# Kernel tuning notes

Hardware: AMD Instinct MI355X
Metric: run time of the kernel (lower is better)

Reference implementation:

```python
import jax, jax.numpy as jnp
import numpy as np

EPS = 1e-3  # kernel epsilon used in Performer generalized kernel
B, H, N, D, M = 1, 8, 1024, 64, 128  # batch, heads, seq, dim_heads, nb_features


def _gaussian_orthogonal_matrix(m, d, seed=0):
    # GaussianOrthogonalRandomMatrix with scaling=0: stacked QR blocks, rows
    # rescaled by chi-distributed norms of gaussian d-vectors.
    rng = np.random.default_rng(seed)
    blocks = []
    for _ in range(m // d):
        g = rng.standard_normal((d, d))
        qmat, _ = np.linalg.qr(g)
        blocks.append(qmat.T)
    proj = np.concatenate(blocks, axis=0)  # [m, d], orthonormal rows per block
    mult = np.linalg.norm(rng.standard_normal((m, d)), axis=1)  # chi norms
    return (mult[:, None] * proj).astype(np.float32)


def setup_inputs() -> dict:
    key = jax.random.key(0)
    kq, kk, kv = jax.random.split(key, 3)
    q = jax.random.normal(kq, (B, H, N, D), dtype=jnp.float32)
    k = jax.random.normal(kk, (B, H, N, D), dtype=jnp.float32)
    v = jax.random.normal(kv, (B, H, N, D), dtype=jnp.float32)
    proj = jnp.asarray(_gaussian_orthogonal_matrix(M, D))
    return {"q": q, "k": k, "v": v, "proj": proj}


def _generalized_kernel(x, proj):
    # kernel_fn(relu)( (x / d**0.25) @ proj^T ) + eps
    normalizer = 1.0 / (x.shape[-1] ** 0.25)
    xp = jnp.einsum('bhnd,md->bhnm', x * normalizer, proj)
    return jax.nn.relu(xp) + EPS


def reference(q, k, v, proj):
    qp = _generalized_kernel(q, proj)  # [B,H,N,M]
    kp = _generalized_kernel(k, proj)  # [B,H,N,M]
    # causal linear attention
    k_cumsum = jnp.cumsum(kp, axis=-2)                              # [B,H,N,M]
    context = jnp.einsum('bhnm,bhne->bhnme', kp, v)                 # [B,H,N,M,D]
    context = jnp.cumsum(context, axis=-3)                          # prefix sums over n
    context = context / k_cumsum[..., None]                         # normalize
    out = jnp.einsum('bhnme,bhnm->bhne', context, qp)               # [B,H,N,D]
    return out
```

## Files before the change

kernel.cpp:

```cpp
#include <hip/hip_runtime.h>

static constexpr int H = 8, N = 1024, D = 64, M = 128, CHUNK = 128, NC = 8;
static constexpr float EPS = 1e-3f;
static constexpr float NORM = 0.35355339059327373f;

typedef __attribute__((ext_vector_type(8))) short short8;
typedef __attribute__((ext_vector_type(4))) float f32x4;

__device__ inline unsigned short f2bf(float x) {
    unsigned u = __float_as_uint(x);
    return (unsigned short)((u + 0x7fffu + ((u >> 16) & 1u)) >> 16);
}
__device__ inline float bf2f(unsigned short u) {
    return __uint_as_float(((unsigned)u) << 16);
}
__device__ inline ushort4 pack4(float4 g) {
    return (ushort4){f2bf(g.x), f2bf(g.y), f2bf(g.z), f2bf(g.w)};
}

__global__ __launch_bounds__(512) void k_projg(const float* __restrict__ q,
                                               const float* __restrict__ k,
                                               const float* __restrict__ proj,
                                               const float* __restrict__ v,
                                               unsigned short* __restrict__ qpb,
                                               unsigned short* __restrict__ kpb,
                                               unsigned short* __restrict__ Gpb,
                                               float* __restrict__ kpart) {
    __shared__ __align__(16) short smem[30208];
    short* projb = smem;
    short* xb = smem + 9216;
    short* obuf = smem + 13824;
    short* kpT = smem + 22528;
    short* vT = smem + 27648;
    const int tid = threadIdx.x;
    const int rblk = blockIdx.x;
    const int h = blockIdx.y;
    const int rowbase = h * N + rblk * 32;
    const int lane = tid & 63, wv = tid >> 6;
    const int rt = wv & 3, mh = wv >> 2;
    const int fr = lane & 15, fq = lane >> 4;

    for (int i4 = tid; i4 < 2048; i4 += 512) {
        int m = i4 >> 4, dq = i4 & 15;
        *(ushort4*)&projb[m * 72 + dq * 4] = pack4(*(const float4*)&proj[i4 * 4]);
    }
    {
        int r = tid >> 4, dq = tid & 15;
        float4 g = *(const float4*)&q[(rowbase + r) * D + dq * 4];
        g.x *= NORM; g.y *= NORM; g.z *= NORM; g.w *= NORM;
        *(ushort4*)&xb[r * 72 + dq * 4] = pack4(g);
        float4 gk = *(const float4*)&k[(rowbase + r) * D + dq * 4];
        gk.x *= NORM; gk.y *= NORM; gk.z *= NORM; gk.w *= NORM;
        *(ushort4*)&xb[(32 + r) * 72 + dq * 4] = pack4(gk);
        int rv = tid & 31, e4 = (tid >> 5) * 4;
        float4 gv = *(const float4*)&v[(rowbase + rv) * D + e4];
        vT[(e4 + 0) * 40 + rv] = (short)f2bf(gv.x);
        vT[(e4 + 1) * 40 + rv] = (short)f2bf(gv.y);
        vT[(e4 + 2) * 40 + rv] = (short)f2bf(gv.z);
        vT[(e4 + 3) * 40 + rv] = (short)f2bf(gv.w);
    }
    __syncthreads();

    f32x4 accp[4];
#pragma unroll
    for (int i = 0; i < 4; i++) accp[i] = (f32x4){0.f, 0.f, 0.f, 0.f};
#pragma unroll
    for (int kt = 0; kt < 2; kt++) {
        short8 a = *(const short8*)&xb[(16 * rt + fr) * 72 + kt * 32 + fq * 8];
#pragma unroll
        for (int i = 0; i < 4; i++) {
            const int mt = mh * 4 + i;
            short8 bb = *(const short8*)&projb[(16 * mt + fr) * 72 + kt * 32 + fq * 8];
            accp[i] = __builtin_amdgcn_mfma_f32_16x16x32_bf16(a, bb, accp[i], 0, 0, 0);
        }
    }
#pragma unroll
    for (int i = 0; i < 4; i++) {
        const int mt = mh * 4 + i;
#pragma unroll
        for (int reg = 0; reg < 4; reg++) {
            const int r = 16 * rt + fq * 4 + reg;
            const int m = 16 * mt + fr;
            unsigned short bv = f2bf(fmaxf(accp[i][reg], 0.f) + EPS);
            obuf[r * 136 + m] = (short)bv;
            if (rt >= 2) kpT[m * 40 + (r - 32)] = (short)bv;
        }
    }
    __syncthreads();

    for (int i = tid; i < 2048; i += 512) {
        int r = i >> 5, cu = i & 31;
        ushort4 val = *(const ushort4*)&obuf[r * 136 + cu * 4];
        unsigned short* g = (r < 32) ? &qpb[(rowbase + r) * M + cu * 4]
                                     : &kpb[(rowbase + r - 32) * M + cu * 4];
        *(ushort4*)g = val;
    }
    const int gb = h * 32 + rblk;
    if (tid < 128) {
        float ks = 0.f;
#pragma unroll 8
        for (int r = 0; r < 32; r++) ks += bf2f((unsigned short)kpT[tid * 40 + r]);
        kpart[gb * M + tid] = ks;
    }
    __syncthreads();

    f32x4 gacc[4];
#pragma unroll
    for (int et = 0; et < 4; et++) gacc[et] = (f32x4){0.f, 0.f, 0.f, 0.f};
    {
        short8 a = *(const short8*)&kpT[(16 * wv + fr) * 40 + fq * 8];
#pragma unroll
        for (int et = 0; et < 4; et++) {
            short8 bb = *(const short8*)&vT[(16 * et + fr) * 40 + fq * 8];
            gacc[et] = __builtin_amdgcn_mfma_f32_16x16x32_bf16(a, bb, gacc[et], 0, 0, 0);
        }
    }
#pragma unroll
    for (int et = 0; et < 4; et++)
#pragma unroll
        for (int reg = 0; reg < 4; reg++) {
            const int m = 16 * wv + fq * 4 + reg;
            obuf[m * 68 + 16 * et + fr] = (short)f2bf(gacc[et][reg]);
        }
    __syncthreads();
    for (int i = tid; i < 2048; i += 512) {
        int m = i >> 4, e4 = (i & 15) * 4;
        *(ushort4*)&Gpb[(gb * M + m) * D + e4] = *(const ushort4*)&obuf[m * 68 + e4];
    }
}

__global__ __launch_bounds__(512) void k_attn(const unsigned short* __restrict__ qpb,
                                              const unsigned short* __restrict__ kpb,
                                              const float* __restrict__ kpart,
                                              const unsigned short* __restrict__ Gpb,
                                              const float* __restrict__ v,
                                              float* __restrict__ out) {
    __shared__ __align__(16) short smem[26112];
    short* bufA = smem;
    short* bufB = smem + 4352;
    short* bufC = smem + 21760;
    short* s0t = bufB;
    short* vT = bufB + 8704;
    const int tid = threadIdx.x;
    const int b = blockIdx.x;
    const int sub = blockIdx.y;
    const int h = b >> 3, c = 7 - (b & 7);
    const int chunkbase = h * N + c * CHUNK;
    const int rowstart = chunkbase + sub * 32;
    const int jrows = (sub + 1) * 32;
    const int lane = tid & 63, wv = tid >> 6;
    const int rt = wv & 1, js = wv >> 1;
    const int fr = lane & 15, fq = lane >> 4;

    float4 vpre[4];
#pragma unroll
    for (int t = 0; t < 4; t++) {
        const int i = tid + t * 512;
        const int j = i >> 4, e4 = (i & 15) * 4;
        vpre[t] = *(const float4*)&v[(chunkbase + j) * D + e4];
    }

    {
        const unsigned int* src = (const unsigned int*)kpb;
        for (int i = tid; i < jrows * 64; i += 512) {
            int j = i >> 6, mu = i & 63;
            ((unsigned int*)&bufB[j * 136])[mu] = src[(chunkbase + j) * 64 + mu];
        }
        const unsigned int* srcq = (const unsigned int*)qpb;
        for (int i = tid; i < 2048; i += 512) {
            int r = i >> 6, mu = i & 63;
            ((unsigned int*)&bufC[r * 136])[mu] = srcq[(rowstart + r) * 64 + mu];
        }
    }
    __syncthreads();

    if (tid < 128) {
        const int m = tid;
        float z = 0.f;
        const int send = c * 4 + sub;
        for (int s = 0; s < send; s++) z += kpart[(h * 32 + s) * M + m];
#pragma unroll 8
        for (int r = 0; r < 32; r++) {
            z += bf2f((unsigned short)bufB[(sub * 32 + r) * 136 + m]);
            bufA[r * 136 + m] = (short)f2bf(
                bf2f((unsigned short)bufC[r * 136 + m]) * __builtin_amdgcn_rcpf(z));
        }
    }
    float s0r[16];
#pragma unroll
    for (int j = 0; j < 16; j++) s0r[j] = 0.f;
    for (int cp = 0; cp < c; cp++) {
#pragma unroll
        for (int p = 0; p < 4; p++) {
            const short* gsrc =
                (const short*)&Gpb[(h * 32 + cp * 4 + p) * (M * D) + tid * 16];
            short8 g0 = *(const short8*)&gsrc[0];
            short8 g1 = *(const short8*)&gsrc[8];
#pragma unroll
            for (int j = 0; j < 8; j++) {
                s0r[j] += bf2f((unsigned short)g0[j]);
                s0r[8 + j] += bf2f((unsigned short)g1[j]);
            }
        }
    }
    __syncthreads();

    const int jtmax = 2 * sub + 2;
    f32x4 acc1[2];
    acc1[0] = (f32x4){0.f, 0.f, 0.f, 0.f};
    acc1[1] = (f32x4){0.f, 0.f, 0.f, 0.f};
#pragma unroll
    for (int kt = 0; kt < 4; kt++) {
        short8 a = *(const short8*)&bufA[(16 * rt + fr) * 136 + kt * 32 + fq * 8];
#pragma unroll
        for (int jl = 0; jl < 2; jl++) {
            const int jt = 2 * js + jl;
            if (jt < jtmax) {
                short8 bb =
                    *(const short8*)&bufB[(16 * jt + fr) * 136 + kt * 32 + fq * 8];
                acc1[jl] =
                    __builtin_amdgcn_mfma_f32_16x16x32_bf16(a, bb, acc1[jl], 0, 0, 0);
            }
        }
    }
    __syncthreads();

#pragma unroll
    for (int jl = 0; jl < 2; jl++) {
        const int jt = 2 * js + jl;
        if (jt < jtmax) {
            const int j = 16 * jt + fr;
#pragma unroll
            for (int reg = 0; reg < 4; reg++) {
                const int nloc = 16 * rt + fq * 4 + reg;
                float val = (j <= sub * 32 + nloc) ? acc1[jl][reg] : 0.f;
                bufC[nloc * 136 + j] = (short)f2bf(val);
            }
        }
    }
    {
        const int m = tid >> 2;
        const int ebase = (tid & 3) * 16;
#pragma unroll
        for (int j = 0; j < 16; j++)
            s0t[(ebase + j) * 136 + m] = (short)f2bf(s0r[j]);
    }
#pragma unroll
    for (int t = 0; t < 4; t++) {
        const int i = tid + t * 512;
        const int j = i >> 4, e4 = (i & 15) * 4;
        vT[(e4 + 0) * 136 + j] = (short)f2bf(vpre[t].x);
        vT[(e4 + 1) * 136 + j] = (short)f2bf(vpre[t].y);
        vT[(e4 + 2) * 136 + j] = (short)f2bf(vpre[t].z);
        vT[(e4 + 3) * 136 + j] = (short)f2bf(vpre[t].w);
    }
    __syncthreads();

    f32x4 acc2 = (f32x4){0.f, 0.f, 0.f, 0.f};
#pragma unroll
    for (int kt = 0; kt < 4; kt++) {
        short8 a = *(const short8*)&bufA[(16 * rt + fr) * 136 + kt * 32 + fq * 8];
        short8 bb = *(const short8*)&s0t[(16 * js + fr) * 136 + kt * 32 + fq * 8];
        acc2 = __builtin_amdgcn_mfma_f32_16x16x32_bf16(a, bb, acc2, 0, 0, 0);
    }
    const int ktmax = sub + 1;
    for (int kt = 0; kt < ktmax; kt++) {
        short8 a = *(const short8*)&bufC[(16 * rt + fr) * 136 + kt * 32 + fq * 8];
        short8 bb = *(const short8*)&vT[(16 * js + fr) * 136 + kt * 32 + fq * 8];
        acc2 = __builtin_amdgcn_mfma_f32_16x16x32_bf16(a, bb, acc2, 0, 0, 0);
    }

#pragma unroll
    for (int reg = 0; reg < 4; reg++) {
        out[(rowstart + 16 * rt + fq * 4 + reg) * D + 16 * js + fr] = acc2[reg];
    }
}

extern "C" void kernel_launch(void* const* d_in, const int* in_sizes, int n_in,
                              void* d_out, int out_size, void* d_ws, size_t ws_size,
                              hipStream_t stream) {
    const float* q = (const float*)d_in[0];
    const float* k = (const float*)d_in[1];
    const float* v = (const float*)d_in[2];
    const float* proj = (const float*)d_in[3];
    float* out = (float*)d_out;

    float* ws = (float*)d_ws;
    float* kpart = ws;
    unsigned short* qpb = (unsigned short*)(kpart + H * 32 * M);
    unsigned short* kpb = qpb + H * N * M;
    unsigned short* Gpb = kpb + H * N * M;

    k_projg<<<dim3(32, H), 512, 0, stream>>>(q, k, proj, v, qpb, kpb, Gpb,
                                             kpart);
    k_attn<<<dim3(H * NC, 4), 512, 0, stream>>>(qpb, kpb, kpart, Gpb, v, out);
}
```

Baseline: 88.22 us.

## Precompute chunk-level prefix sums of G and k-normalizer in a separate kernel

Adds a k_prefix kernel that computes exclusive prefix sums over chunks of the partial context matrices G and the k cumsum partials once per head. k_attn then loads a single precomputed S0 and z value instead of each block re-summing up to 28 G partials and kpart rows. This removes the redundant per-block reduction work and its global reads, which were heaviest for late chunks. The cost is an extra kernel launch and a round trip through workspace memory, and the prefix is now rounded to bf16 once.

```diff
diff --git a/kernel.cpp b/kernel.cpp
--- a/kernel.cpp
+++ b/kernel.cpp
@@ -129,10 +129,44 @@
     }
 }
 
+__global__ __launch_bounds__(256) void k_prefix(const float* __restrict__ kpart,
+                                                const unsigned short* __restrict__ Gpb,
+                                                float* __restrict__ zpre,
+                                                unsigned short* __restrict__ S0pre) {
+    const int h = blockIdx.x >> 3, oct = blockIdx.x & 7;
+    const int tid = threadIdx.x;
+    const int eb = oct * 1024 + tid * 4;
+    float a0 = 0.f, a1 = 0.f, a2 = 0.f, a3 = 0.f;
+#pragma unroll
+    for (int c = 0; c < 8; c++) {
+        ushort4 w = {f2bf(a0), f2bf(a1), f2bf(a2), f2bf(a3)};
+        *(ushort4*)&S0pre[(h * 8 + c) * (M * D) + eb] = w;
+#pragma unroll
+        for (int p = 0; p < 4; p++) {
+            ushort4 g = *(const ushort4*)&Gpb[(h * 32 + c * 4 + p) * (M * D) + eb];
+            a0 += bf2f(g.x);
+            a1 += bf2f(g.y);
+            a2 += bf2f(g.z);
+            a3 += bf2f(g.w);
+        }
+    }
+    if (oct == 0 && tid < 128) {
+        float vals[32];
+#pragma unroll
+        for (int s = 0; s < 32; s++) vals[s] = kpart[(h * 32 + s) * M + tid];
+        float z = 0.f;
+#pragma unroll
+        for (int s = 0; s < 32; s++) {
+            zpre[(h * 32 + s) * M + tid] = z;
+            z += vals[s];
+        }
+    }
+}
+
 __global__ __launch_bounds__(512) void k_attn(const unsigned short* __restrict__ qpb,
                                               const unsigned short* __restrict__ kpb,
-                                              const float* __restrict__ kpart,
-                                              const unsigned short* __restrict__ Gpb,
+                                              const float* __restrict__ zpre,
+                                              const unsigned short* __restrict__ S0pre,
                                               const float* __restrict__ v,
                                               float* __restrict__ out) {
     __shared__ __align__(16) short smem[26112];
@@ -159,6 +193,11 @@
         const int j = i >> 4, e4 = (i & 15) * 4;
         vpre[t] = *(const float4*)&v[(chunkbase + j) * D + e4];
     }
+    const int pm = tid >> 2, peb = (tid & 3) * 16;
+    short8 s0a = *(const short8*)&S0pre[(h * 8 + c) * (M * D) + pm * D + peb];
+    short8 s0b = *(const short8*)&S0pre[(h * 8 + c) * (M * D) + pm * D + peb + 8];
+    float zinit = 0.f;
+    if (tid < 128) zinit = zpre[(h * 32 + c * 4 + sub) * M + tid];
 
     {
         const unsigned int* src = (const unsigned int*)kpb;
@@ -176,31 +215,12 @@
 
     if (tid < 128) {
         const int m = tid;
-        float z = 0.f;
-        const int send = c * 4 + sub;
-        for (int s = 0; s < send; s++) z += kpart[(h * 32 + s) * M + m];
+        float z = zinit;
 #pragma unroll 8
         for (int r = 0; r < 32; r++) {
             z += bf2f((unsigned short)bufB[(sub * 32 + r) * 136 + m]);
             bufA[r * 136 + m] = (short)f2bf(
                 bf2f((unsigned short)bufC[r * 136 + m]) * __builtin_amdgcn_rcpf(z));
-        }
-    }
-    float s0r[16];
-#pragma unroll
-    for (int j = 0; j < 16; j++) s0r[j] = 0.f;
-    for (int cp = 0; cp < c; cp++) {
-#pragma unroll
-        for (int p = 0; p < 4; p++) {
-            const short* gsrc =
-                (const short*)&Gpb[(h * 32 + cp * 4 + p) * (M * D) + tid * 16];
-            short8 g0 = *(const short8*)&gsrc[0];
-            short8 g1 = *(const short8*)&gsrc[8];
-#pragma unroll
-            for (int j = 0; j < 8; j++) {
-                s0r[j] += bf2f((unsigned short)g0[j]);
-                s0r[8 + j] += bf2f((unsigned short)g1[j]);
-            }
         }
     }
     __syncthreads();
@@ -239,11 +259,11 @@
         }
     }
     {
-        const int m = tid >> 2;
-        const int ebase = (tid & 3) * 16;
-#pragma unroll
-        for (int j = 0; j < 16; j++)
-            s0t[(ebase + j) * 136 + m] = (short)f2bf(s0r[j]);
+#pragma unroll
+        for (int j = 0; j < 8; j++) {
+            s0t[(peb + j) * 136 + pm] = s0a[j];
+            s0t[(peb + 8 + j) * 136 + pm] = s0b[j];
+        }
     }
 #pragma unroll
     for (int t = 0; t < 4; t++) {
@@ -290,8 +310,11 @@
     unsigned short* qpb = (unsigned short*)(kpart + H * 32 * M);
     unsigned short* kpb = qpb + H * N * M;
     unsigned short* Gpb = kpb + H * N * M;
+    float* zpre = (float*)(Gpb + H * 32 * M * D);
+    unsigned short* S0pre = (unsigned short*)(zpre + H * 32 * M);
 
     k_projg<<<dim3(32, H), 512, 0, stream>>>(q, k, proj, v, qpb, kpb, Gpb,
                                              kpart);
-    k_attn<<<dim3(H * NC, 4), 512, 0, stream>>>(qpb, kpb, kpart, Gpb, v, out);
-}
+    k_prefix<<<dim3(64), 256, 0, stream>>>(kpart, Gpb, zpre, S0pre);
+    k_attn<<<dim3(H * NC, 4), 512, 0, stream>>>(qpb, kpb, zpre, S0pre, v, out);
+}
```

Result: faster. 81.16 us (-8.0%).
